# Kernel tuning notes

Hardware: AMD Instinct MI355X
Metric: run time of the kernel (lower is better)

Reference implementation:

```python
import jax, jax.numpy as jnp
import numpy as np

E = 8          # num experts
TOPK = 2
D = 1024       # emb_size (expert hidden == emb_size)


def setup_inputs() -> dict:
    key = jax.random.key(0)
    ks = jax.random.split(key, 8)
    s = 1.0 / np.sqrt(D)
    x = jax.random.normal(ks[0], (4, 1024, D), dtype=jnp.float32)
    gate_W = jax.random.uniform(ks[1], (E, D), jnp.float32, -s, s)   # torch Linear weight (out,in)
    gate_b = jax.random.uniform(ks[2], (E,), jnp.float32, -s, s)
    w1 = jax.random.uniform(ks[3], (E, D, D), jnp.float32, -s, s)    # per-expert first Linear (out,in)
    b1 = jax.random.uniform(ks[4], (E, D), jnp.float32, -s, s)
    w2 = jax.random.uniform(ks[5], (E, D, D), jnp.float32, -s, s)    # per-expert second Linear (out,in)
    b2 = jax.random.uniform(ks[6], (E, D), jnp.float32, -s, s)
    return {"x": x, "gate_W": gate_W, "gate_b": gate_b,
            "w1": w1, "b1": b1, "w2": w2, "b2": b2}


def reference(x, gate_W, gate_b, w1, b1, w2, b2):
    x_shape = x.shape
    xt = x.reshape(-1, x_shape[-1])                       # [N, D]

    # gating
    gate_logits = xt @ gate_W.T + gate_b                  # [N, E]
    gate_prob = jax.nn.softmax(gate_logits, axis=-1)      # [N, E]
    top_w, top_i = jax.lax.top_k(gate_prob, TOPK)         # [N, K]
    top_w = jax.nn.softmax(top_w, axis=-1)                # renormalize over top-k

    # dense per-expert MLP: h = relu(x @ W1^T + b1); o = h @ W2^T + b2
    h = jax.nn.relu(jnp.einsum('nd,ehd->neh', xt, w1) + b1[None])   # [N, E, D]
    o = jnp.einsum('neh,eoh->neo', h, w2) + b2[None]                # [N, E, D]

    # gather top-k expert outputs per token and combine with weights
    o_top = jnp.take_along_axis(o, top_i[:, :, None], axis=1)       # [N, K, D]
    y = jnp.sum(o_top * top_w[:, :, None], axis=1)                  # [N, D]

    return y.reshape(x_shape), gate_prob
```

## Files before the change

### kernel.cpp

```cpp
#include <hip/hip_runtime.h>

#define NTOK 4096
#define DIM 1024
#define NE 8
#define NPAIR (NTOK * 2)
#define CVT_BLOCKS 16384
#define GATE_BLOCKS (NTOK / 4)

typedef __bf16 bf16x8 __attribute__((ext_vector_type(8)));
typedef float floatx4 __attribute__((ext_vector_type(4)));

__device__ __forceinline__ unsigned short f2bf(float f) {
  unsigned u = __float_as_uint(f);
  u = u + 0x7fffu + ((u >> 16) & 1u);
  return (unsigned short)(u >> 16);
}
__device__ __forceinline__ float bf2f(unsigned short h) {
  return __uint_as_float(((unsigned)h) << 16);
}

__device__ __forceinline__ void gld_lds16(const unsigned short* g, unsigned short* l) {
  __builtin_amdgcn_global_load_lds(
      (const __attribute__((address_space(1))) void*)g,
      (__attribute__((address_space(3))) void*)l, 16, 0, 0);
}

__global__ __launch_bounds__(256) void prep_kernel(
    const float4* __restrict__ w1, ushort4* __restrict__ w1_bf,
    const float4* __restrict__ w2, ushort4* __restrict__ w2_bf,
    const float* __restrict__ x, const float* __restrict__ gW,
    const float* __restrict__ gb,
    float* __restrict__ gp_out, int2* __restrict__ tops,
    float* __restrict__ pairw, int* __restrict__ cnt, int* __restrict__ done,
    unsigned short* __restrict__ x_bf)
{
  const int tid = threadIdx.x;
  int b = blockIdx.x;
  if (b < CVT_BLOCKS) {
    const float4* src = w1;
    ushort4* dst = w1_bf;
    if (b >= CVT_BLOCKS / 2) { b -= CVT_BLOCKS / 2; src = w2; dst = w2_bf; }
    const int i = b * 256 + tid;
    float4 v = src[i];
    ushort4 o;
    o.x = f2bf(v.x); o.y = f2bf(v.y); o.z = f2bf(v.z); o.w = f2bf(v.w);
    dst[i] = o;
    return;
  }
  b -= CVT_BLOCKS;
  if (b == 0) {
    if (tid < NE) cnt[tid] = 0;
    if (tid == NE) *done = 0;
  }
  const int lane = tid & 63;
  const int wid = tid >> 6;
  const int t = b * 4 + wid;

  float4 xv[4];
#pragma unroll
  for (int j = 0; j < 4; j++)
    xv[j] = ((const float4*)(x + (size_t)t * DIM))[lane + 64 * j];

#pragma unroll
  for (int j = 0; j < 4; j++) {
    ushort4 o;
    o.x = f2bf(xv[j].x); o.y = f2bf(xv[j].y);
    o.z = f2bf(xv[j].z); o.w = f2bf(xv[j].w);
    ((ushort4*)(x_bf + (size_t)t * DIM))[lane + 64 * j] = o;
  }

  float p[NE];
#pragma unroll
  for (int e = 0; e < NE; e++) {
    const float4* gwe = (const float4*)(gW + e * DIM);
    float s = 0.f;
#pragma unroll
    for (int j = 0; j < 4; j++) {
      float4 g = gwe[lane + 64 * j];
      s += xv[j].x * g.x + xv[j].y * g.y + xv[j].z * g.z + xv[j].w * g.w;
    }
    p[e] = s;
  }
#pragma unroll
  for (int e = 0; e < NE; e++) {
#pragma unroll
    for (int off = 32; off >= 1; off >>= 1) p[e] += __shfl_xor(p[e], off);
  }

  float m = -1e30f;
#pragma unroll
  for (int e = 0; e < NE; e++) { p[e] += gb[e]; m = fmaxf(m, p[e]); }
  float s = 0.f;
  float pr[NE];
#pragma unroll
  for (int e = 0; e < NE; e++) { pr[e] = __expf(p[e] - m); s += pr[e]; }
  float inv = 1.f / s;
#pragma unroll
  for (int e = 0; e < NE; e++) pr[e] *= inv;

  if (lane < NE) gp_out[(size_t)t * NE + lane] = pr[lane];

  if (lane == 0) {
    int i0 = 0;
#pragma unroll
    for (int e = 1; e < NE; e++) if (pr[e] > pr[i0]) i0 = e;
    int i1 = (i0 == 0) ? 1 : 0;
#pragma unroll
    for (int e = 0; e < NE; e++) if (e != i0 && pr[e] > pr[i1]) i1 = e;
    float d = __expf(pr[i1] - pr[i0]);
    float w0 = 1.f / (1.f + d);
    tops[t] = make_int2(i0, i1);
    pairw[t * 2] = w0;
    pairw[t * 2 + 1] = 1.f - w0;
  }
}

__global__ __launch_bounds__(256) void bin_sched_kernel(
    const int2* __restrict__ tops, int* __restrict__ cnt,
    int* __restrict__ bucket,
    int* __restrict__ posmap,
    int* __restrict__ done, int* __restrict__ base,
    int* __restrict__ sched, int* __restrict__ sched_n)
{
  const int t = blockIdx.x * 256 + threadIdx.x;
  const int lane = threadIdx.x & 63;
  int2 ti = tops[t];
#pragma unroll
  for (int slot = 0; slot < 2; slot++) {
    int e = slot ? ti.y : ti.x;
#pragma unroll
    for (int ex = 0; ex < NE; ex++) {
      bool mine = (e == ex);
      unsigned long long mask = __ballot(mine);
      if (mask) {
        int leader = __ffsll((long long)mask) - 1;
        int total = __popcll(mask);
        int prefix = __popcll(mask & ((1ull << lane) - 1ull));
        int idx = 0;
        if (lane == leader) idx = atomicAdd(&cnt[ex], total);
        idx = __shfl(idx, leader) + prefix;
        if (mine) {
          bucket[ex * NTOK + idx] = t * 2 + slot;
          posmap[t * 2 + slot] = (ex << 16) | idx;
        }
      }
    }
  }
  __syncthreads();
  if (threadIdx.x == 0) {
    if (atomicAdd(done, 1) == gridDim.x - 1) {
      int b = 0, pos = 0;
      for (int e = 0; e < NE; e++) {
        int c = atomicAdd(&cnt[e], 0);
        base[e] = b;
        int tiles = (c + 127) >> 7;
        for (int i = 0; i < tiles; i++) {
          int valid = c - i * 128; if (valid > 128) valid = 128;
          sched[pos++] = (e << 20) | (i << 8) | valid;
        }
        b += c;
      }
      base[NE] = b;
      *sched_n = pos;
    }
  }
}

template <int RELU, int GATHER>
__global__ __launch_bounds__(256) void ffn_gemm(
    const unsigned short* __restrict__ A,
    const unsigned short* __restrict__ B,
    const float* __restrict__ bias,
    const int* __restrict__ base,
    const int* __restrict__ bucket,
    const int* __restrict__ sched, const int* __restrict__ sched_n,
    unsigned short* __restrict__ Out)
{
  const int l = blockIdx.x;
  const int xcd = l & 7;
  const int w = l >> 3;
  const int nt = w & 7;
  const int slot = xcd * 9 + (w >> 3);
  if (slot >= *sched_n) return;
  const int se = sched[slot];
  const int e = se >> 20;
  const int mt = (se >> 8) & 0xfff;
  const int valid = se & 255;
  const int arow0 = base[e] + mt * 128;

  __shared__ unsigned short lda[128 * 64];
  __shared__ unsigned short ldb[128 * 64];

  const int tid = threadIdx.x;
  const int lane = tid & 63;
  const int wid = tid >> 6;

  const unsigned short* ap[4];
  const unsigned short* bp[4];
#pragma unroll
  for (int j = 0; j < 4; j++) {
    int g = wid * 4 + j;
    int row = g * 8 + (lane >> 3);
    int gran = (lane & 7) ^ (row & 7);
    if (GATHER) {
      int idx = mt * 128 + row;
      int ce = base[e + 1] - base[e];
      if (idx > ce - 1) idx = ce - 1;
      int tok = bucket[e * NTOK + idx] >> 1;
      ap[j] = A + (size_t)tok * DIM + (gran << 3);
    } else {
      int prow = arow0 + row;
      if (prow > NPAIR - 1) prow = NPAIR - 1;
      ap[j] = A + (size_t)prow * DIM + (gran << 3);
    }
    bp[j] = B + ((size_t)e * DIM + nt * 128 + row) * DIM + (gran << 3);
  }

  floatx4 acc[4][4] = {};
  const int wm = (wid & 1) * 64;
  const int wn = (wid >> 1) * 64;
  const int quad = lane >> 4;
  const int cl = lane & 15;
  const int sw = cl & 7;

  for (int k0 = 0; k0 < 16; k0++) {
#pragma unroll
    for (int j = 0; j < 4; j++) {
      int g = wid * 4 + j;
      gld_lds16(ap[j], &lda[g * 512]);
      gld_lds16(bp[j], &ldb[g * 512]);
      ap[j] += 64;
      bp[j] += 64;
    }
    __syncthreads();
#pragma unroll
    for (int kk = 0; kk < 64; kk += 32) {
      const int gb = (kk >> 3) + quad;
      const int goff = ((gb ^ sw) << 3);
      bf16x8 af[4], bfr[4];
#pragma unroll
      for (int mi = 0; mi < 4; mi++)
        af[mi] = *(const bf16x8*)&lda[(wm + mi * 16 + cl) * 64 + goff];
#pragma unroll
      for (int ni = 0; ni < 4; ni++)
        bfr[ni] = *(const bf16x8*)&ldb[(wn + ni * 16 + cl) * 64 + goff];
#pragma unroll
      for (int mi = 0; mi < 4; mi++)
#pragma unroll
        for (int ni = 0; ni < 4; ni++)
          acc[mi][ni] = __builtin_amdgcn_mfma_f32_16x16x32_bf16(af[mi], bfr[ni], acc[mi][ni], 0, 0, 0);
    }
    if (k0 < 15) __syncthreads();
  }

#pragma unroll
  for (int ni = 0; ni < 4; ni++) {
    int col = nt * 128 + wn + ni * 16 + cl;
    float bval = bias[e * DIM + col];
#pragma unroll
    for (int mi = 0; mi < 4; mi++) {
#pragma unroll
      for (int reg = 0; reg < 4; reg++) {
        int rl = wm + mi * 16 + quad * 4 + reg;
        if (rl < valid) {
          float v = acc[mi][ni][reg] + bval;
          if (RELU) v = fmaxf(v, 0.f);
          Out[(size_t)(arow0 + rl) * DIM + col] = f2bf(v);
        }
      }
    }
  }
}

__global__ __launch_bounds__(256) void combine_kernel(
    const unsigned short* __restrict__ o, const int* __restrict__ posmap,
    const int* __restrict__ base, const float* __restrict__ pairw,
    float* __restrict__ y)
{
  const int t = blockIdx.x;
  const int tid = threadIdx.x;
  const int pm0 = posmap[t * 2], pm1 = posmap[t * 2 + 1];
  const int p0 = base[pm0 >> 16] + (pm0 & 0xffff);
  const int p1 = base[pm1 >> 16] + (pm1 & 0xffff);
  const float w0 = pairw[t * 2], w1 = pairw[t * 2 + 1];
  ushort4 a = ((const ushort4*)(o + (size_t)p0 * DIM))[tid];
  ushort4 b = ((const ushort4*)(o + (size_t)p1 * DIM))[tid];
  float4 r;
  r.x = w0 * bf2f(a.x) + w1 * bf2f(b.x);
  r.y = w0 * bf2f(a.y) + w1 * bf2f(b.y);
  r.z = w0 * bf2f(a.z) + w1 * bf2f(b.z);
  r.w = w0 * bf2f(a.w) + w1 * bf2f(b.w);
  ((float4*)(y + (size_t)t * DIM))[tid] = r;
}

extern "C" void kernel_launch(void* const* d_in, const int* in_sizes, int n_in,
                              void* d_out, int out_size, void* d_ws, size_t ws_size,
                              hipStream_t stream) {
  const float* x  = (const float*)d_in[0];
  const float* gW = (const float*)d_in[1];
  const float* gb = (const float*)d_in[2];
  const float* w1 = (const float*)d_in[3];
  const float* b1 = (const float*)d_in[4];
  const float* w2 = (const float*)d_in[5];
  const float* b2 = (const float*)d_in[6];
  float* y  = (float*)d_out;
  float* gp = (float*)d_out + (size_t)NTOK * DIM;

  char* ws = (char*)d_ws;
  unsigned short* x_bf   = (unsigned short*)(ws);
  unsigned short* w2_bf  = (unsigned short*)(ws + (size_t)(8u << 20));
  unsigned short* h_pack = (unsigned short*)(ws + (size_t)(24u << 20));
  unsigned short* w1_bf  = (unsigned short*)(ws + (size_t)(40u << 20));
  unsigned short* o_pack = (unsigned short*)(ws + (size_t)(40u << 20));
  char* tail = ws + (size_t)(56u << 20);
  int*   cnt     = (int*)(tail);
  int*   done    = cnt + NE;
  int*   base    = done + 1;
  int*   sched   = base + NE + 1;
  int*   sched_n = sched + 256;
  int*   bucket  = sched_n + 1;
  float* pairw   = (float*)(bucket + NE * NTOK);
  int2*  tops    = (int2*)(pairw + NPAIR);
  int*   posmap  = (int*)(tops + NTOK);

  const int gemm_grid = 576;
  prep_kernel<<<CVT_BLOCKS + GATE_BLOCKS, 256, 0, stream>>>(
      (const float4*)w1, (ushort4*)w1_bf, (const float4*)w2, (ushort4*)w2_bf,
      x, gW, gb, gp, tops, pairw, cnt, done, x_bf);
  bin_sched_kernel<<<NTOK / 256, 256, 0, stream>>>(tops, cnt, bucket, posmap, done,
                                                   base, sched, sched_n);
  ffn_gemm<1, 1><<<gemm_grid, 256, 0, stream>>>(x_bf, w1_bf, b1, base, bucket, sched, sched_n, h_pack);
  ffn_gemm<0, 0><<<gemm_grid, 256, 0, stream>>>(h_pack, w2_bf, b2, base, bucket, sched, sched_n, o_pack);
  combine_kernel<<<NTOK, 256, 0, stream>>>(o_pack, posmap, base, pairw, y);
}
```

Baseline: 228.9 us.

## Fuse top-k combine into second GEMM via atomics; reuse w1 buffer for w2

Removes the combine kernel and the bf16 o_pack intermediate. The second expert GEMM now scales each output row by its routing weight and atomically adds it into y, which is zeroed in the prep kernel. The w2 conversion moves into its own kernel launched after the first GEMM, so w2_bf can share w1_bf's buffer, shrinking the workspace. The cost is float atomics on every output element, with contention from two experts per token, a non-deterministic summation order, and one extra kernel launch.

```diff
diff --git a/kernel.cpp b/kernel.cpp
--- a/kernel.cpp
+++ b/kernel.cpp
@@ -4,8 +4,10 @@
 #define DIM 1024
 #define NE 8
 #define NPAIR (NTOK * 2)
-#define CVT_BLOCKS 16384
 #define GATE_BLOCKS (NTOK / 4)
+#define CVT_BLOCKS 8192
+#define NBIN (NTOK / 256)
+#define GRID 576
 
 typedef __bf16 bf16x8 __attribute__((ext_vector_type(8)));
 typedef float floatx4 __attribute__((ext_vector_type(4)));
@@ -27,31 +29,23 @@
 
 __global__ __launch_bounds__(256) void prep_kernel(
     const float4* __restrict__ w1, ushort4* __restrict__ w1_bf,
-    const float4* __restrict__ w2, ushort4* __restrict__ w2_bf,
     const float* __restrict__ x, const float* __restrict__ gW,
-    const float* __restrict__ gb,
-    float* __restrict__ gp_out, int2* __restrict__ tops,
-    float* __restrict__ pairw, int* __restrict__ cnt, int* __restrict__ done,
-    unsigned short* __restrict__ x_bf)
+    const float* __restrict__ gb, float* __restrict__ gp_out,
+    int2* __restrict__ tops, float* __restrict__ pairw,
+    int* __restrict__ cnt, unsigned short* __restrict__ x_bf,
+    float* __restrict__ y)
 {
   const int tid = threadIdx.x;
   int b = blockIdx.x;
-  if (b < CVT_BLOCKS) {
-    const float4* src = w1;
-    ushort4* dst = w1_bf;
-    if (b >= CVT_BLOCKS / 2) { b -= CVT_BLOCKS / 2; src = w2; dst = w2_bf; }
-    const int i = b * 256 + tid;
-    float4 v = src[i];
+  if (b >= GATE_BLOCKS) {
+    const int i = (b - GATE_BLOCKS) * 256 + tid;
+    float4 v = w1[i];
     ushort4 o;
     o.x = f2bf(v.x); o.y = f2bf(v.y); o.z = f2bf(v.z); o.w = f2bf(v.w);
-    dst[i] = o;
+    w1_bf[i] = o;
     return;
   }
-  b -= CVT_BLOCKS;
-  if (b == 0) {
-    if (tid < NE) cnt[tid] = 0;
-    if (tid == NE) *done = 0;
-  }
+  if (b == 0 && tid < NE + 1) cnt[tid] = 0;
   const int lane = tid & 63;
   const int wid = tid >> 6;
   const int t = b * 4 + wid;
@@ -61,8 +55,10 @@
   for (int j = 0; j < 4; j++)
     xv[j] = ((const float4*)(x + (size_t)t * DIM))[lane + 64 * j];
 
+  const float4 z4 = make_float4(0.f, 0.f, 0.f, 0.f);
 #pragma unroll
   for (int j = 0; j < 4; j++) {
+    ((float4*)(y + (size_t)t * DIM))[lane + 64 * j] = z4;
     ushort4 o;
     o.x = f2bf(xv[j].x); o.y = f2bf(xv[j].y);
     o.z = f2bf(xv[j].z); o.w = f2bf(xv[j].w);
@@ -166,15 +162,27 @@
   }
 }
 
-template <int RELU, int GATHER>
+__global__ __launch_bounds__(256) void cvt_kernel(
+    const float4* __restrict__ src, ushort4* __restrict__ dst)
+{
+  const int i = blockIdx.x * 256 + threadIdx.x;
+  float4 v = src[i];
+  ushort4 o;
+  o.x = f2bf(v.x); o.y = f2bf(v.y); o.z = f2bf(v.z); o.w = f2bf(v.w);
+  dst[i] = o;
+}
+
+template <int RELU, int GATHER, int ATOMIC>
 __global__ __launch_bounds__(256) void ffn_gemm(
     const unsigned short* __restrict__ A,
     const unsigned short* __restrict__ B,
     const float* __restrict__ bias,
     const int* __restrict__ base,
     const int* __restrict__ bucket,
+    const float* __restrict__ pairw,
     const int* __restrict__ sched, const int* __restrict__ sched_n,
-    unsigned short* __restrict__ Out)
+    unsigned short* __restrict__ Out,
+    float* __restrict__ yout)
 {
   const int l = blockIdx.x;
   const int xcd = l & 7;
@@ -253,44 +261,46 @@
     if (k0 < 15) __syncthreads();
   }
 
-#pragma unroll
-  for (int ni = 0; ni < 4; ni++) {
-    int col = nt * 128 + wn + ni * 16 + cl;
-    float bval = bias[e * DIM + col];
+  if (ATOMIC) {
+    float bval[4];
+#pragma unroll
+    for (int ni = 0; ni < 4; ni++) bval[ni] = bias[e * DIM + nt * 128 + wn + ni * 16 + cl];
 #pragma unroll
     for (int mi = 0; mi < 4; mi++) {
 #pragma unroll
       for (int reg = 0; reg < 4; reg++) {
         int rl = wm + mi * 16 + quad * 4 + reg;
         if (rl < valid) {
-          float v = acc[mi][ni][reg] + bval;
-          if (RELU) v = fmaxf(v, 0.f);
-          Out[(size_t)(arow0 + rl) * DIM + col] = f2bf(v);
+          int pairid = bucket[e * NTOK + mt * 128 + rl];
+          float wgt = pairw[pairid];
+          float* yrow = yout + (size_t)(pairid >> 1) * DIM + nt * 128 + wn;
+#pragma unroll
+          for (int ni = 0; ni < 4; ni++) {
+            float v = acc[mi][ni][reg] + bval[ni];
+            atomicAdd(&yrow[ni * 16 + cl], wgt * v);
+          }
         }
       }
     }
-  }
-}
-
-__global__ __launch_bounds__(256) void combine_kernel(
-    const unsigned short* __restrict__ o, const int* __restrict__ posmap,
-    const int* __restrict__ base, const float* __restrict__ pairw,
-    float* __restrict__ y)
-{
-  const int t = blockIdx.x;
-  const int tid = threadIdx.x;
-  const int pm0 = posmap[t * 2], pm1 = posmap[t * 2 + 1];
-  const int p0 = base[pm0 >> 16] + (pm0 & 0xffff);
-  const int p1 = base[pm1 >> 16] + (pm1 & 0xffff);
-  const float w0 = pairw[t * 2], w1 = pairw[t * 2 + 1];
-  ushort4 a = ((const ushort4*)(o + (size_t)p0 * DIM))[tid];
-  ushort4 b = ((const ushort4*)(o + (size_t)p1 * DIM))[tid];
-  float4 r;
-  r.x = w0 * bf2f(a.x) + w1 * bf2f(b.x);
-  r.y = w0 * bf2f(a.y) + w1 * bf2f(b.y);
-  r.z = w0 * bf2f(a.z) + w1 * bf2f(b.z);
-  r.w = w0 * bf2f(a.w) + w1 * bf2f(b.w);
-  ((float4*)(y + (size_t)t * DIM))[tid] = r;
+  } else {
+#pragma unroll
+    for (int ni = 0; ni < 4; ni++) {
+      int col = nt * 128 + wn + ni * 16 + cl;
+      float bval = bias[e * DIM + col];
+#pragma unroll
+      for (int mi = 0; mi < 4; mi++) {
+#pragma unroll
+        for (int reg = 0; reg < 4; reg++) {
+          int rl = wm + mi * 16 + quad * 4 + reg;
+          if (rl < valid) {
+            float v = acc[mi][ni][reg] + bval;
+            if (RELU) v = fmaxf(v, 0.f);
+            Out[(size_t)(arow0 + rl) * DIM + col] = f2bf(v);
+          }
+        }
+      }
+    }
+  }
 }
 
 extern "C" void kernel_launch(void* const* d_in, const int* in_sizes, int n_in,
@@ -308,11 +318,10 @@
 
   char* ws = (char*)d_ws;
   unsigned short* x_bf   = (unsigned short*)(ws);
+  unsigned short* w1_bf  = (unsigned short*)(ws + (size_t)(8u << 20));
   unsigned short* w2_bf  = (unsigned short*)(ws + (size_t)(8u << 20));
   unsigned short* h_pack = (unsigned short*)(ws + (size_t)(24u << 20));
-  unsigned short* w1_bf  = (unsigned short*)(ws + (size_t)(40u << 20));
-  unsigned short* o_pack = (unsigned short*)(ws + (size_t)(40u << 20));
-  char* tail = ws + (size_t)(56u << 20);
+  char* tail = ws + (size_t)(40u << 20);
   int*   cnt     = (int*)(tail);
   int*   done    = cnt + NE;
   int*   base    = done + 1;
@@ -323,13 +332,13 @@
   int2*  tops    = (int2*)(pairw + NPAIR);
   int*   posmap  = (int*)(tops + NTOK);
 
-  const int gemm_grid = 576;
-  prep_kernel<<<CVT_BLOCKS + GATE_BLOCKS, 256, 0, stream>>>(
-      (const float4*)w1, (ushort4*)w1_bf, (const float4*)w2, (ushort4*)w2_bf,
-      x, gW, gb, gp, tops, pairw, cnt, done, x_bf);
-  bin_sched_kernel<<<NTOK / 256, 256, 0, stream>>>(tops, cnt, bucket, posmap, done,
-                                                   base, sched, sched_n);
-  ffn_gemm<1, 1><<<gemm_grid, 256, 0, stream>>>(x_bf, w1_bf, b1, base, bucket, sched, sched_n, h_pack);
-  ffn_gemm<0, 0><<<gemm_grid, 256, 0, stream>>>(h_pack, w2_bf, b2, base, bucket, sched, sched_n, o_pack);
-  combine_kernel<<<NTOK, 256, 0, stream>>>(o_pack, posmap, base, pairw, y);
-}
+  prep_kernel<<<GATE_BLOCKS + CVT_BLOCKS, 256, 0, stream>>>(
+      (const float4*)w1, (ushort4*)w1_bf, x, gW, gb, gp, tops, pairw, cnt, x_bf, y);
+  bin_sched_kernel<<<NBIN, 256, 0, stream>>>(tops, cnt, bucket, posmap, done,
+                                             base, sched, sched_n);
+  ffn_gemm<1, 1, 0><<<GRID, 256, 0, stream>>>(x_bf, w1_bf, b1, base, bucket, pairw,
+                                              sched, sched_n, h_pack, nullptr);
+  cvt_kernel<<<CVT_BLOCKS, 256, 0, stream>>>((const float4*)w2, (ushort4*)w2_bf);
+  ffn_gemm<0, 0, 1><<<GRID, 256, 0, stream>>>(h_pack, w2_bf, b2, base, bucket, pairw,
+                                              sched, sched_n, nullptr, y);
+}
```

New measurement: 237.4 us. 1.04x slower.
